# Optimization experiments

Measured on AMD Instinct MI355X. Metric: run time of the kernel, lower is better.

## Reference

```python
import jax, jax.numpy as jnp
import numpy as np

N_NODES = 50000
N_EDGES = 600000
IN_DIM = 128
OUT_DIM = 128
N_REL = 32
N_BASES = 4
BN_EPS = 1e-5


def setup_inputs() -> dict:
    key = jax.random.key(0)
    ks = jax.random.split(key, 8)
    entity_emb = jax.random.normal(ks[0], (N_NODES, IN_DIM), dtype=jnp.float32)
    bases = jax.random.normal(ks[1], (N_BASES, IN_DIM, OUT_DIM), dtype=jnp.float32) * 0.05
    coefficients = jax.random.normal(ks[2], (N_REL, N_BASES), dtype=jnp.float32) * 0.5
    W_loop = jax.random.normal(ks[3], (IN_DIM, OUT_DIM), dtype=jnp.float32) * 0.05
    b_loop = jnp.zeros((OUT_DIM,), dtype=jnp.float32)
    gamma = jnp.ones((OUT_DIM,), dtype=jnp.float32)
    beta = jnp.zeros((OUT_DIM,), dtype=jnp.float32)
    edge_index = jax.random.randint(ks[4], (2, N_EDGES), 0, N_NODES, dtype=jnp.int32)
    edge_type = jax.random.randint(ks[5], (N_EDGES,), 0, N_REL, dtype=jnp.int32)
    return {"entity_emb": entity_emb, "bases": bases, "coefficients": coefficients,
            "W_loop": W_loop, "b_loop": b_loop, "gamma": gamma, "beta": beta,
            "edge_index": edge_index, "edge_type": edge_type}


def reference(entity_emb, bases, coefficients, W_loop, b_loop, gamma, beta, edge_index, edge_type):
    N = entity_emb.shape[0]
    # self-loop linear
    out = entity_emb @ W_loop + b_loop  # [N, out_dim]
    # basis decomposition: per-relation weight W[r] = sum_b coeff[r,b] * bases[b]
    W = jnp.einsum('rb,bio->rio', coefficients, bases)  # [R, in, out]
    src, dst = edge_index[0], edge_index[1]
    # per-edge message: entity_emb[src_e] @ W[edge_type_e]  (vectorizes the per-relation loop)
    msg = jnp.einsum('ei,eio->eo', entity_emb[src], W[edge_type])  # [E, out]
    out = out + jax.ops.segment_sum(msg, dst, num_segments=N)
    # degree normalization (in-degree over all edges, clamped at 1)
    deg = jax.ops.segment_sum(jnp.ones_like(dst, dtype=out.dtype), dst, num_segments=N)
    out = out / jnp.maximum(deg, 1.0)[:, None]
    # BatchNorm1d (training mode: biased batch stats over node dim)
    mean = jnp.mean(out, axis=0)
    var = jnp.mean((out - mean) ** 2, axis=0)
    out = (out - mean) / jnp.sqrt(var + BN_EPS) * gamma + beta
    return jax.nn.relu(out)
```

## Files before the change

kernel.cpp:

```cpp
#include <hip/hip_runtime.h>
#include <cstdint>

#define NN 50000
#define NE 600000
#define NPAIRS 1563
#define GSTRIDE 512

typedef unsigned short ushort_t;
typedef __bf16 bf16_t;
typedef __attribute__((ext_vector_type(8))) bf16_t bf16x8;
typedef __attribute__((ext_vector_type(8))) ushort_t ushort8;
typedef __attribute__((ext_vector_type(4))) float f32x4;
typedef __attribute__((ext_vector_type(2))) float f32x2;

#define WT_OFF   0ul
#define XG_OFF   40960ul
#define XBF_OFF  16040960ul
#define CNT_OFF  19240960ul
#define CUR_OFF  19290960ul
#define BSUM_OFF 19340960ul
#define BSCN_OFF 19341088ul
#define CS_OFF   19341216ul
#define CSQ_OFF  19341344ul

__device__ __forceinline__ float2 bf2_to_f2(uint32_t u) {
    float2 r;
    r.x = __uint_as_float(u << 16);
    r.y = __uint_as_float(u & 0xffff0000u);
    return r;
}

__device__ __forceinline__ ushort_t f2bf(float f) {
    uint32_t u = __float_as_uint(f);
    u = (u + 0x7fffu + ((u >> 16) & 1u)) >> 16;
    return (ushort_t)u;
}

__device__ __forceinline__ uint32_t f2bf2(float x, float y) {
    return (uint32_t)f2bf(x) | ((uint32_t)f2bf(y) << 16);
}

__device__ __forceinline__ void async_copy16(const void* g, void* l) {
    __builtin_amdgcn_global_load_lds(
        (const __attribute__((address_space(1))) void*)g,
        (__attribute__((address_space(3))) void*)l, 16, 0, 0);
}

__global__ __launch_bounds__(256) void k_prep(
    const float* __restrict__ Wl, const float* __restrict__ bases,
    ushort_t* __restrict__ WT)
{
    const int i = blockIdx.x * 256 + threadIdx.x;
    if (i >= 128 * 640) return;
    const int n = i / 640;
    const int kk = i - n * 640;
    float v;
    if (kk < 128) v = Wl[kk * 128 + n];
    else {
        const int j = kk - 128;
        v = bases[(size_t)(j >> 7) * 16384 + (j & 127) * 128 + n];
    }
    WT[i] = f2bf(v);
}

__global__ __launch_bounds__(256) void k_cast(
    const float* __restrict__ X, ushort_t* __restrict__ Xbf,
    ushort_t* __restrict__ XG)
{
    __shared__ ushort_t L[16][136];
    const int tid = threadIdx.x;
    const int tile = blockIdx.x;
    {
        const int row = tid >> 4, gc = tid & 15;
        const int node = tile * 16 + row;
        const float4* p = (const float4*)(X + (size_t)node * 128 + gc * 8);
        const float4 a = p[0], b = p[1];
        ushort_t t8[8] = { f2bf(a.x), f2bf(a.y), f2bf(a.z), f2bf(a.w),
                           f2bf(b.x), f2bf(b.y), f2bf(b.z), f2bf(b.w) };
        const uint4 v = *(const uint4*)t8;
        *(uint4*)&L[row][gc * 8] = v;
        *(uint4*)(Xbf + (size_t)node * 128 + gc * 8) = v;
    }
    __syncthreads();
    {
        const int g = tid >> 4, r2 = tid & 15;
        const uint4 u = *(const uint4*)&L[r2][g * 8];
        *(uint4*)(XG + (size_t)tile * 10240 + g * 128 + r2 * 8) = u;
    }
}

__global__ __launch_bounds__(256) void k_hist(
    const int* __restrict__ eidx, int* __restrict__ cnt)
{
    const int* __restrict__ dst = eidx + NE;
    for (int e = blockIdx.x * 256 + threadIdx.x; e < NE; e += gridDim.x * 256)
        atomicAdd(cnt + dst[e], 1);
}

__global__ __launch_bounds__(256) void k_scan1(
    const int* __restrict__ cnt, int* __restrict__ curs, int* __restrict__ bsum)
{
    __shared__ int sh[256];
    const int tid = threadIdx.x;
    const int i0 = blockIdx.x * 512 + tid * 2;
    const int v0 = (i0 < NN) ? cnt[i0] : 0;
    const int v1 = (i0 + 1 < NN) ? cnt[i0 + 1] : 0;
    int s = v0 + v1;
    sh[tid] = s;
    __syncthreads();
#pragma unroll
    for (int off = 1; off < 256; off <<= 1) {
        int t = (tid >= off) ? sh[tid - off] : 0;
        __syncthreads();
        sh[tid] += t;
        __syncthreads();
    }
    const int excl = sh[tid] - s;
    if (i0 < NN) curs[i0] = excl;
    if (i0 + 1 < NN) curs[i0 + 1] = excl + v0;
    if (tid == 255) bsum[blockIdx.x] = sh[255];
}

__global__ __launch_bounds__(128) void k_scan2(
    const int* __restrict__ bsum, int* __restrict__ bscan, int nblk)
{
    __shared__ int sh[128];
    const int tid = threadIdx.x;
    int v = (tid < nblk) ? bsum[tid] : 0;
    sh[tid] = v;
    __syncthreads();
#pragma unroll
    for (int off = 1; off < 128; off <<= 1) {
        int t = (tid >= off) ? sh[tid - off] : 0;
        __syncthreads();
        sh[tid] += t;
        __syncthreads();
    }
    if (tid < nblk) bscan[tid] = sh[tid] - v;
}

__global__ __launch_bounds__(256) void k_scan3(
    int* __restrict__ curs, const int* __restrict__ bscan)
{
    const int add = bscan[blockIdx.x];
    const int i0 = blockIdx.x * 512 + threadIdx.x * 2;
    if (i0 < NN) curs[i0] += add;
    if (i0 + 1 < NN) curs[i0 + 1] += add;
}

__global__ __launch_bounds__(256) void k_scatter(
    const int* __restrict__ eidx, const int* __restrict__ etype,
    int* __restrict__ curs, uint32_t* __restrict__ epack)
{
    const int* __restrict__ src = eidx;
    const int* __restrict__ dst = eidx + NE;
    for (int e = blockIdx.x * 256 + threadIdx.x; e < NE; e += gridDim.x * 256) {
        const int d = dst[e];
        const int pos = atomicAdd(curs + d, 1);
        epack[pos] = (uint32_t)src[e] | ((uint32_t)etype[e] << 16);
    }
}

__device__ __forceinline__ void accum_pk(
    const uint4 xv, const float4 cw, f32x2* m2)
{
    f32x2 x2[4];
    float2 p;
    p = bf2_to_f2(xv.x); x2[0] = f32x2{p.x, p.y};
    p = bf2_to_f2(xv.y); x2[1] = f32x2{p.x, p.y};
    p = bf2_to_f2(xv.z); x2[2] = f32x2{p.x, p.y};
    p = bf2_to_f2(xv.w); x2[3] = f32x2{p.x, p.y};
#pragma unroll
    for (int c2 = 0; c2 < 4; ++c2) {
        m2[0 * 4 + c2] += cw.x * x2[c2];
        m2[1 * 4 + c2] += cw.y * x2[c2];
        m2[2 * 4 + c2] += cw.z * x2[c2];
        m2[3 * 4 + c2] += cw.w * x2[c2];
    }
}

__global__ __launch_bounds__(256, 4) void k_gather(
    const ushort_t* __restrict__ Xbf, const uint32_t* __restrict__ epack,
    const int* __restrict__ cnt, const int* __restrict__ curs,
    const float* __restrict__ coeff, ushort_t* __restrict__ XG)
{
    const int lane = threadIdx.x & 63;
    const int w = threadIdx.x >> 6;
    const int sub = lane >> 4;
    const int k = lane & 15;
    const int tile = blockIdx.x;
    const int d = tile * 16 + w * 4 + sub;

    const int n = cnt[d];
    const int end = curs[d];
    int j = end - n;

    f32x2 m2[16];
#pragma unroll
    for (int i = 0; i < 16; ++i) m2[i] = f32x2{0.f, 0.f};

    for (; j + 7 < end; j += 8) {
        uint32_t ep[8];
#pragma unroll
        for (int i = 0; i < 8; ++i) ep[i] = epack[j + i];
        uint4 xv[8];
        float4 cw[8];
#pragma unroll
        for (int i = 0; i < 8; ++i) {
            const int s = ep[i] & 0xffff;
            const int t = ep[i] >> 16;
            xv[i] = *(const uint4*)(Xbf + (size_t)s * 128 + k * 8);
            cw[i] = *(const float4*)(coeff + t * 4);
        }
#pragma unroll
        for (int i = 0; i < 8; ++i) accum_pk(xv[i], cw[i], m2);
    }
    if (j + 3 < end) {
        uint32_t ep[4];
#pragma unroll
        for (int i = 0; i < 4; ++i) ep[i] = epack[j + i];
        uint4 xv[4];
        float4 cw[4];
#pragma unroll
        for (int i = 0; i < 4; ++i) {
            const int s = ep[i] & 0xffff;
            const int t = ep[i] >> 16;
            xv[i] = *(const uint4*)(Xbf + (size_t)s * 128 + k * 8);
            cw[i] = *(const float4*)(coeff + t * 4);
        }
#pragma unroll
        for (int i = 0; i < 4; ++i) accum_pk(xv[i], cw[i], m2);
        j += 4;
    }
    for (; j < end; ++j) {
        const uint32_t ep = epack[j];
        const int s = ep & 0xffff;
        const int t = ep >> 16;
        const uint4 xv = *(const uint4*)(Xbf + (size_t)s * 128 + k * 8);
        const float4 cw = *(const float4*)(coeff + t * 4);
        accum_pk(xv, cw, m2);
    }

    uint32_t* gb = (uint32_t*)(XG + (size_t)tile * 10240);
#pragma unroll
    for (int b = 0; b < 4; ++b) {
        uint4 v;
        v.x = f2bf2(m2[b * 4 + 0][0], m2[b * 4 + 0][1]);
        v.y = f2bf2(m2[b * 4 + 1][0], m2[b * 4 + 1][1]);
        v.z = f2bf2(m2[b * 4 + 2][0], m2[b * 4 + 2][1]);
        v.w = f2bf2(m2[b * 4 + 3][0], m2[b * 4 + 3][1]);
        *(uint4*)(gb + (16 + b * 16 + k) * 64 + (w * 4 + sub) * 4) = v;
    }
}

__global__ __launch_bounds__(256, 2) void k_gemm_f(
    const ushort_t* __restrict__ XG, const ushort_t* __restrict__ WT,
    const float* __restrict__ bl, const int* __restrict__ cnt,
    float* __restrict__ out, float* __restrict__ colsum,
    float* __restrict__ colsq)
{
    __shared__ ushort_t As[2][2][10240];
    const int tid = threadIdx.x;
    const int lane = tid & 63;
    const int w = tid >> 6;
    const int m = lane & 15;
    const int quad = lane >> 4;

    auto stage = [&](int buf, int pr) {
        const ushort_t* base = XG + (size_t)pr * 20480;
#pragma unroll
        for (int j = 0; j < 10; ++j) {
            const int idx = w * 10 + j;
            const int tl = idx / 20;
            const int off = idx - tl * 20;
            async_copy16(base + (size_t)tl * 10240 + off * 512 + lane * 8,
                         &As[buf][tl][off * 512]);
        }
    };

    int p = blockIdx.x;
    stage(0, p);

    const ushort_t* bp0 = WT + (size_t)(w * 32 + m) * 640 + quad * 8;
    const ushort_t* bp1 = bp0 + 16 * 640;
    ushort8 B0[20], B1[20];
#pragma unroll
    for (int c = 0; c < 20; ++c) {
        B0[c] = *(const ushort8*)(bp0 + c * 32);
        B1[c] = *(const ushort8*)(bp1 + c * 32);
    }
    const float blv0 = bl[w * 32 + m];
    const float blv1 = bl[w * 32 + 16 + m];
    float s0 = 0.f, q0 = 0.f, s1 = 0.f, q1 = 0.f;

    __syncthreads();

    int buf = 0;
    while (p < NPAIRS) {
        const int pn = p + GSTRIDE;
        if (pn < NPAIRS) stage(buf ^ 1, pn);

        f32x4 cc[2][2];
#pragma unroll
        for (int rt = 0; rt < 2; ++rt)
#pragma unroll
            for (int ct = 0; ct < 2; ++ct)
#pragma unroll
                for (int i = 0; i < 4; ++i) cc[rt][ct][i] = 0.f;

#pragma unroll
        for (int c = 0; c < 20; ++c) {
            const int aoff = (c * 4 + quad) * 128 + m * 8;
            const bf16x8 a0 = __builtin_bit_cast(bf16x8, *(const ushort8*)&As[buf][0][aoff]);
            const bf16x8 a1 = __builtin_bit_cast(bf16x8, *(const ushort8*)&As[buf][1][aoff]);
            const bf16x8 b0 = __builtin_bit_cast(bf16x8, B0[c]);
            const bf16x8 b1 = __builtin_bit_cast(bf16x8, B1[c]);
            cc[0][0] = __builtin_amdgcn_mfma_f32_16x16x32_bf16(a0, b0, cc[0][0], 0, 0, 0);
            cc[0][1] = __builtin_amdgcn_mfma_f32_16x16x32_bf16(a0, b1, cc[0][1], 0, 0, 0);
            cc[1][0] = __builtin_amdgcn_mfma_f32_16x16x32_bf16(a1, b0, cc[1][0], 0, 0, 0);
            cc[1][1] = __builtin_amdgcn_mfma_f32_16x16x32_bf16(a1, b1, cc[1][1], 0, 0, 0);
        }

        const int row0 = p * 32;
#pragma unroll
        for (int rt = 0; rt < 2; ++rt) {
            const int rowb = row0 + rt * 16 + quad * 4;
#pragma unroll
            for (int r = 0; r < 4; ++r) {
                const int row = rowb + r;
                if (row < NN) {
                    const int dg = cnt[row];
                    const float inv = 1.0f / (float)((dg > 0) ? dg : 1);
                    float* po = out + (size_t)row * 128 + w * 32 + m;
                    const float v0 = (cc[rt][0][r] + blv0) * inv;
                    const float v1 = (cc[rt][1][r] + blv1) * inv;
                    po[0]  = v0;
                    po[16] = v1;
                    s0 += v0; q0 += v0 * v0;
                    s1 += v1; q1 += v1 * v1;
                }
            }
        }

        if (pn < NPAIRS) __syncthreads();
        buf ^= 1;
        p = pn;
    }

    s0 += __shfl_down(s0, 32); q0 += __shfl_down(q0, 32);
    s0 += __shfl_down(s0, 16); q0 += __shfl_down(q0, 16);
    s1 += __shfl_down(s1, 32); q1 += __shfl_down(q1, 32);
    s1 += __shfl_down(s1, 16); q1 += __shfl_down(q1, 16);
    if (lane < 16) {
        atomicAdd(colsum + w * 32 + lane, s0);
        atomicAdd(colsq  + w * 32 + lane, q0);
        atomicAdd(colsum + w * 32 + 16 + lane, s1);
        atomicAdd(colsq  + w * 32 + 16 + lane, q1);
    }
}

__global__ __launch_bounds__(256) void k_bn_relu(
    float* __restrict__ out, const float* __restrict__ colsum,
    const float* __restrict__ colsq, const float* __restrict__ gamma,
    const float* __restrict__ beta)
{
    __shared__ float sc[128], sh[128];
    const int tid = threadIdx.x;
    if (tid < 128) {
        const float mean = colsum[tid] * (1.0f / NN);
        const float var = colsq[tid] * (1.0f / NN) - mean * mean;
        const float g = gamma[tid] * rsqrtf(var + 1e-5f);
        sc[tid] = g;
        sh[tid] = beta[tid] - mean * g;
    }
    __syncthreads();
    const int total = NN * 32;
    for (int i = blockIdx.x * 256 + tid; i < total; i += gridDim.x * 256) {
        const int c = (i & 31) << 2;
        float4 v = *(float4*)(out + (size_t)i * 4);
        v.x = fmaxf(fmaf(v.x, sc[c + 0], sh[c + 0]), 0.f);
        v.y = fmaxf(fmaf(v.y, sc[c + 1], sh[c + 1]), 0.f);
        v.z = fmaxf(fmaf(v.z, sc[c + 2], sh[c + 2]), 0.f);
        v.w = fmaxf(fmaf(v.w, sc[c + 3], sh[c + 3]), 0.f);
        *(float4*)(out + (size_t)i * 4) = v;
    }
}

extern "C" void kernel_launch(void* const* d_in, const int* in_sizes, int n_in,
                              void* d_out, int out_size, void* d_ws, size_t ws_size,
                              hipStream_t stream)
{
    const float* X      = (const float*)d_in[0];
    const float* bases  = (const float*)d_in[1];
    const float* coeff  = (const float*)d_in[2];
    const float* Wl     = (const float*)d_in[3];
    const float* bl     = (const float*)d_in[4];
    const float* gamma  = (const float*)d_in[5];
    const float* beta   = (const float*)d_in[6];
    const int*   eidx   = (const int*)d_in[7];
    const int*   etype  = (const int*)d_in[8];
    float* out = (float*)d_out;

    float* ws = (float*)d_ws;
    ushort_t* WT     = (ushort_t*)(ws + WT_OFF);
    ushort_t* XG     = (ushort_t*)(ws + XG_OFF);
    ushort_t* Xbf    = (ushort_t*)(ws + XBF_OFF);
    int*      cnt    = (int*)(ws + CNT_OFF);
    int*      curs   = (int*)(ws + CUR_OFF);
    int*      bsum   = (int*)(ws + BSUM_OFF);
    int*      bscan  = (int*)(ws + BSCN_OFF);
    float*    colsum = ws + CS_OFF;
    float*    colsq  = ws + CSQ_OFF;
    uint32_t* epack  = (uint32_t*)d_out;

    hipMemsetAsync(cnt, 0, (CSQ_OFF + 128 - CNT_OFF) * sizeof(float), stream);

    const int nblk_scan = (NN + 511) / 512;

    k_prep<<<(128 * 640 + 255) / 256, 256, 0, stream>>>(Wl, bases, WT);
    k_cast<<<3125, 256, 0, stream>>>(X, Xbf, XG);
    k_hist<<<2048, 256, 0, stream>>>(eidx, cnt);
    k_scan1<<<nblk_scan, 256, 0, stream>>>(cnt, curs, bsum);
    k_scan2<<<1, 128, 0, stream>>>(bsum, bscan, nblk_scan);
    k_scan3<<<nblk_scan, 256, 0, stream>>>(curs, bscan);
    k_scatter<<<2048, 256, 0, stream>>>(eidx, etype, curs, epack);
    k_gather<<<3125, 256, 0, stream>>>(Xbf, epack, cnt, curs, coeff, XG);
    k_gemm_f<<<GSTRIDE, 256, 0, stream>>>(XG, WT, bl, cnt, out, colsum, colsq);
    k_bn_relu<<<1024, 256, 0, stream>>>(out, colsum, colsq, gamma, beta);
}
```

Measured before the change: 249.9 us.

## Fuse prep, cast and histogram kernels; GEMM reads self-loop operand from Xbf directly

Merges the weight-transpose, bf16 cast and degree-histogram kernels into one launch using block-index ranges. The cast no longer writes a transposed copy of X into the GEMM staging buffer. Instead the GEMM stage gathers the self-loop slice straight from the row-major Xbf array with per-lane addressing, and the gather output buffer shrinks to the aggregated-basis part only. This removes two launches and about 3 MB of redundant writes, at the cost of less contiguous async loads for the self-loop part of the GEMM A tile.

Result: faster. 243.9 us (-2.4%).

```diff
diff --git a/kernel.cpp b/kernel.cpp
--- a/kernel.cpp
+++ b/kernel.cpp
@@ -14,14 +14,14 @@
 typedef __attribute__((ext_vector_type(2))) float f32x2;
 
 #define WT_OFF   0ul
-#define XG_OFF   40960ul
-#define XBF_OFF  16040960ul
-#define CNT_OFF  19240960ul
-#define CUR_OFF  19290960ul
-#define BSUM_OFF 19340960ul
-#define BSCN_OFF 19341088ul
-#define CS_OFF   19341216ul
-#define CSQ_OFF  19341344ul
+#define XGG_OFF  40960ul
+#define XBF_OFF  12845056ul
+#define CNT_OFF  16046080ul
+#define CUR_OFF  16096080ul
+#define BSUM_OFF 16146080ul
+#define BSCN_OFF 16146208ul
+#define CS_OFF   16146336ul
+#define CSQ_OFF  16146464ul
 
 __device__ __forceinline__ float2 bf2_to_f2(uint32_t u) {
     float2 r;
@@ -46,55 +46,39 @@
         (__attribute__((address_space(3))) void*)l, 16, 0, 0);
 }
 
-__global__ __launch_bounds__(256) void k_prep(
-    const float* __restrict__ Wl, const float* __restrict__ bases,
-    ushort_t* __restrict__ WT)
-{
-    const int i = blockIdx.x * 256 + threadIdx.x;
-    if (i >= 128 * 640) return;
-    const int n = i / 640;
-    const int kk = i - n * 640;
-    float v;
-    if (kk < 128) v = Wl[kk * 128 + n];
-    else {
-        const int j = kk - 128;
-        v = bases[(size_t)(j >> 7) * 16384 + (j & 127) * 128 + n];
-    }
-    WT[i] = f2bf(v);
-}
-
-__global__ __launch_bounds__(256) void k_cast(
-    const float* __restrict__ X, ushort_t* __restrict__ Xbf,
-    ushort_t* __restrict__ XG)
-{
-    __shared__ ushort_t L[16][136];
+__global__ __launch_bounds__(256) void k_pre(
+    const float* __restrict__ X, const float* __restrict__ Wl,
+    const float* __restrict__ bases, const int* __restrict__ eidx,
+    ushort_t* __restrict__ WT, ushort_t* __restrict__ Xbf,
+    int* __restrict__ cnt)
+{
+    const int b = blockIdx.x;
     const int tid = threadIdx.x;
-    const int tile = blockIdx.x;
-    {
+    if (b < 320) {
+        const int i = b * 256 + tid;
+        const int n = i / 640;
+        const int kk = i - n * 640;
+        float v;
+        if (kk < 128) v = Wl[kk * 128 + n];
+        else {
+            const int j = kk - 128;
+            v = bases[(size_t)(j >> 7) * 16384 + (j & 127) * 128 + n];
+        }
+        WT[i] = f2bf(v);
+    } else if (b < 3445) {
+        const int tile = b - 320;
         const int row = tid >> 4, gc = tid & 15;
         const int node = tile * 16 + row;
         const float4* p = (const float4*)(X + (size_t)node * 128 + gc * 8);
-        const float4 a = p[0], b = p[1];
+        const float4 a = p[0], c = p[1];
         ushort_t t8[8] = { f2bf(a.x), f2bf(a.y), f2bf(a.z), f2bf(a.w),
-                           f2bf(b.x), f2bf(b.y), f2bf(b.z), f2bf(b.w) };
-        const uint4 v = *(const uint4*)t8;
-        *(uint4*)&L[row][gc * 8] = v;
-        *(uint4*)(Xbf + (size_t)node * 128 + gc * 8) = v;
-    }
-    __syncthreads();
-    {
-        const int g = tid >> 4, r2 = tid & 15;
-        const uint4 u = *(const uint4*)&L[r2][g * 8];
-        *(uint4*)(XG + (size_t)tile * 10240 + g * 128 + r2 * 8) = u;
-    }
-}
-
-__global__ __launch_bounds__(256) void k_hist(
-    const int* __restrict__ eidx, int* __restrict__ cnt)
-{
-    const int* __restrict__ dst = eidx + NE;
-    for (int e = blockIdx.x * 256 + threadIdx.x; e < NE; e += gridDim.x * 256)
-        atomicAdd(cnt + dst[e], 1);
+                           f2bf(c.x), f2bf(c.y), f2bf(c.z), f2bf(c.w) };
+        *(uint4*)(Xbf + (size_t)node * 128 + gc * 8) = *(const uint4*)t8;
+    } else {
+        const int* __restrict__ dst = eidx + NE;
+        for (int e = (b - 3445) * 256 + tid; e < NE; e += 2048 * 256)
+            atomicAdd(cnt + dst[e], 1);
+    }
 }
 
 __global__ __launch_bounds__(256) void k_scan1(
@@ -182,7 +166,7 @@
 __global__ __launch_bounds__(256, 4) void k_gather(
     const ushort_t* __restrict__ Xbf, const uint32_t* __restrict__ epack,
     const int* __restrict__ cnt, const int* __restrict__ curs,
-    const float* __restrict__ coeff, ushort_t* __restrict__ XG)
+    const float* __restrict__ coeff, ushort_t* __restrict__ XG_G)
 {
     const int lane = threadIdx.x & 63;
     const int w = threadIdx.x >> 6;
@@ -241,7 +225,7 @@
         accum_pk(xv, cw, m2);
     }
 
-    uint32_t* gb = (uint32_t*)(XG + (size_t)tile * 10240);
+    uint32_t* gb = (uint32_t*)(XG_G + (size_t)tile * 8192);
 #pragma unroll
     for (int b = 0; b < 4; ++b) {
         uint4 v;
@@ -249,15 +233,15 @@
         v.y = f2bf2(m2[b * 4 + 1][0], m2[b * 4 + 1][1]);
         v.z = f2bf2(m2[b * 4 + 2][0], m2[b * 4 + 2][1]);
         v.w = f2bf2(m2[b * 4 + 3][0], m2[b * 4 + 3][1]);
-        *(uint4*)(gb + (16 + b * 16 + k) * 64 + (w * 4 + sub) * 4) = v;
+        *(uint4*)(gb + (b * 16 + k) * 64 + (w * 4 + sub) * 4) = v;
     }
 }
 
 __global__ __launch_bounds__(256, 2) void k_gemm_f(
-    const ushort_t* __restrict__ XG, const ushort_t* __restrict__ WT,
-    const float* __restrict__ bl, const int* __restrict__ cnt,
-    float* __restrict__ out, float* __restrict__ colsum,
-    float* __restrict__ colsq)
+    const ushort_t* __restrict__ XG_G, const ushort_t* __restrict__ WT,
+    const ushort_t* __restrict__ Xbf, const float* __restrict__ bl,
+    const int* __restrict__ cnt, float* __restrict__ out,
+    float* __restrict__ colsum, float* __restrict__ colsq)
 {
     __shared__ ushort_t As[2][2][10240];
     const int tid = threadIdx.x;
@@ -267,14 +251,21 @@
     const int quad = lane >> 4;
 
     auto stage = [&](int buf, int pr) {
-        const ushort_t* base = XG + (size_t)pr * 20480;
 #pragma unroll
         for (int j = 0; j < 10; ++j) {
             const int idx = w * 10 + j;
             const int tl = idx / 20;
             const int off = idx - tl * 20;
-            async_copy16(base + (size_t)tl * 10240 + off * 512 + lane * 8,
-                         &As[buf][tl][off * 512]);
+            const int tile = pr * 2 + tl;
+            const ushort_t* src;
+            if (off < 4) {
+                const int node = tile * 16 + (lane & 15);
+                const int g = off * 4 + (lane >> 4);
+                src = Xbf + (size_t)node * 128 + g * 8;
+            } else {
+                src = XG_G + (size_t)tile * 8192 + (off - 4) * 512 + lane * 8;
+            }
+            async_copy16(src, &As[buf][tl][off * 512]);
         }
     };
 
@@ -403,7 +394,7 @@
 
     float* ws = (float*)d_ws;
     ushort_t* WT     = (ushort_t*)(ws + WT_OFF);
-    ushort_t* XG     = (ushort_t*)(ws + XG_OFF);
+    ushort_t* XG_G   = (ushort_t*)(ws + XGG_OFF);
     ushort_t* Xbf    = (ushort_t*)(ws + XBF_OFF);
     int*      cnt    = (int*)(ws + CNT_OFF);
     int*      curs   = (int*)(ws + CUR_OFF);
@@ -417,14 +408,13 @@
 
     const int nblk_scan = (NN + 511) / 512;
 
-    k_prep<<<(128 * 640 + 255) / 256, 256, 0, stream>>>(Wl, bases, WT);
-    k_cast<<<3125, 256, 0, stream>>>(X, Xbf, XG);
-    k_hist<<<2048, 256, 0, stream>>>(eidx, cnt);
+    k_pre<<<5493, 256, 0, stream>>>(X, Wl, bases, eidx, WT, Xbf, cnt);
     k_scan1<<<nblk_scan, 256, 0, stream>>>(cnt, curs, bsum);
     k_scan2<<<1, 128, 0, stream>>>(bsum, bscan, nblk_scan);
     k_scan3<<<nblk_scan, 256, 0, stream>>>(curs, bscan);
     k_scatter<<<2048, 256, 0, stream>>>(eidx, etype, curs, epack);
-    k_gather<<<3125, 256, 0, stream>>>(Xbf, epack, cnt, curs, coeff, XG);
-    k_gemm_f<<<GSTRIDE, 256, 0, stream>>>(XG, WT, bl, cnt, out, colsum, colsq);
+    k_gather<<<3125, 256, 0, stream>>>(Xbf, epack, cnt, curs, coeff, XG_G);
+    k_gemm_f<<<GSTRIDE, 256, 0, stream>>>(XG_G, WT, Xbf, bl, cnt,
+                                          out, colsum, colsq);
     k_bn_relu<<<1024, 256, 0, stream>>>(out, colsum, colsq, gamma, beta);
 }
```
